# Kernel optimization log

Measured on AMD Instinct MI355X. Metric: run time of the kernel, lower is better.

Reference implementation:

```python
import jax, jax.numpy as jnp
import numpy as np

TEMPERATURE = 8.0  # sqrt(head_dim=64)
NEG_INF = -1000000000.0


def setup_inputs() -> dict:
    key = jax.random.key(0)
    kq, kk, kv, km = jax.random.split(key, 4)
    B, H, S, D = 2, 16, 2048, 64
    q = jax.random.normal(kq, (B, H, S, D), dtype=jnp.float32)
    k = jax.random.normal(kk, (B, H, S, D), dtype=jnp.float32)
    v = jax.random.normal(kv, (B, H, S, D), dtype=jnp.float32)
    mask = jax.random.randint(km, (B, 1, S, S), 0, 2, dtype=jnp.int32)
    return {"q": q, "k": k, "v": v, "mask": mask}


def reference(q, k, v, mask):
    # scores: [B,H,S,S] = (q/T) @ k^T
    attn = jnp.einsum('bhqd,bhkd->bhqk', q / TEMPERATURE, k)
    attn = jnp.where(mask == 0, NEG_INF, attn)
    attn = jax.nn.softmax(attn, axis=-1)  # dropout is identity in eval mode
    output = jnp.einsum('bhqk,bhkd->bhqd', attn, v)
    return (output, attn)
```

## Files before the change

### kernel.cpp

```cpp
#include <hip/hip_runtime.h>
#include <hip/hip_bf16.h>


using short4v = __attribute__((ext_vector_type(4))) short;
using short8v = __attribute__((ext_vector_type(8))) short;
using float4v = __attribute__((ext_vector_type(4))) float;

#define S_LEN 2048
#define D_DIM 64
#define QT 64
#define KTILE 64
#define NIT (S_LEN / KTILE)
#define NW (S_LEN / 64)
#define LDK 72
#define ATTN_OFF (2 * 16 * 2048 * 64)

__device__ __forceinline__ short f2bf(float x) {
  __hip_bfloat16 h = __float2bfloat16(x);
  return __builtin_bit_cast(short, h);
}
__device__ __forceinline__ float bf2f(short s) {
  return __builtin_bit_cast(float, ((unsigned)(unsigned short)s) << 16);
}

__global__ __launch_bounds__(256) void pack_mask_kernel(
    const int* __restrict__ mask, unsigned long long* __restrict__ pm, int nwords) {
  const int lane = threadIdx.x & 63;
  int gw = (blockIdx.x * blockDim.x + threadIdx.x) >> 6;
  const int stride = (gridDim.x * blockDim.x) >> 6;
  for (int w = gw; w < nwords; w += stride) {
    int m = mask[(size_t)w * 64 + lane];
    unsigned long long bits = __ballot(m != 0);
    if (lane == 0) pm[w] = bits;
  }
}

template <bool PACKED>
__global__ __launch_bounds__(256, 4) void sdpa_kernel(
    const float* __restrict__ q, const float* __restrict__ k,
    const float* __restrict__ v, const int* __restrict__ mask,
    const unsigned long long* __restrict__ pm, float* __restrict__ out) {
  __shared__ short lds_k[KTILE * LDK];
  __shared__ short lds_vt[D_DIM * LDK];
  __shared__ short lds_p[QT * LDK];

  const int tid  = threadIdx.x;
  const int wave = tid >> 6;
  const int lane = tid & 63;
  const int quad = lane >> 4;
  const int l16  = lane & 15;

  const int blk = blockIdx.x;
  const int qt  = blk & (NIT - 1);
  const int bh  = blk >> 5;
  const int b   = bh >> 4;

  const float* qp = q + (size_t)bh * S_LEN * D_DIM;
  const float* kp = k + (size_t)bh * S_LEN * D_DIM;
  const float* vp = v + (size_t)bh * S_LEN * D_DIM;
  const int*   mp = mask + (size_t)b * S_LEN * S_LEN;
  float* outO = out + (size_t)bh * S_LEN * D_DIM;
  float* outA = out + (size_t)ATTN_OFF + (size_t)bh * S_LEN * S_LEN;

  const int qbase = qt * QT;
  const int qrowC = qbase + wave * 16 + quad * 4;

  const float QSCALE = 0.18033688011112042f;
  short8v qa[2];
  {
    const int qrow = qbase + wave * 16 + l16;
    const float* src = qp + (size_t)qrow * D_DIM + quad * 8;
#pragma unroll
    for (int c = 0; c < 2; ++c) {
      float4v x0 = *(const float4v*)(src + c * 32);
      float4v x1 = *(const float4v*)(src + c * 32 + 4);
      short8v t;
      t[0] = f2bf(x0[0] * QSCALE); t[1] = f2bf(x0[1] * QSCALE);
      t[2] = f2bf(x0[2] * QSCALE); t[3] = f2bf(x0[3] * QSCALE);
      t[4] = f2bf(x1[0] * QSCALE); t[5] = f2bf(x1[1] * QSCALE);
      t[6] = f2bf(x1[2] * QSCALE); t[7] = f2bf(x1[3] * QSCALE);
      qa[c] = t;
    }
  }

  float lsum[4] = {0.f, 0.f, 0.f, 0.f};

#pragma unroll 1
  for (int kt = 0; kt < NIT; ++kt) {
#pragma unroll
    for (int i = 0; i < 4; ++i) {
      int f = tid + i * 256;
      int row = f >> 4;
      int col = (f & 15) * 4;
      float4v x = *(const float4v*)(kp + (size_t)(kt * KTILE + row) * D_DIM + col);
      short4v y;
      y[0] = f2bf(x[0]); y[1] = f2bf(x[1]); y[2] = f2bf(x[2]); y[3] = f2bf(x[3]);
      *(short4v*)(lds_k + row * LDK + col) = y;
    }
    __syncthreads();

    unsigned long long mrow[4];
    if (PACKED) {
#pragma unroll
      for (int r = 0; r < 4; ++r)
        mrow[r] = pm[((size_t)b * S_LEN + qrowC + r) * NW + kt];
    }
#pragma unroll
    for (int t = 0; t < 4; ++t) {
      float4v acc = {0.f, 0.f, 0.f, 0.f};
#pragma unroll
      for (int c = 0; c < 2; ++c) {
        short8v bf = *(const short8v*)(lds_k + (t * 16 + l16) * LDK + c * 32 + quad * 8);
        acc = __builtin_amdgcn_mfma_f32_16x16x32_bf16(qa[c], bf, acc, 0, 0, 0);
      }
      const int kcol = kt * KTILE + t * 16 + l16;
#pragma unroll
      for (int r = 0; r < 4; ++r) {
        bool mv = PACKED ? (((mrow[r] >> (t * 16 + l16)) & 1ull) != 0)
                         : (mp[(size_t)(qrowC + r) * S_LEN + kcol] != 0);
        float p = mv ? exp2f(acc[r]) : 0.f;
        lsum[r] += p;
      }
    }
    __syncthreads();
  }

  float invl[4];
#pragma unroll
  for (int r = 0; r < 4; ++r) {
    float s = lsum[r];
    s += __shfl_xor(s, 1);
    s += __shfl_xor(s, 2);
    s += __shfl_xor(s, 4);
    s += __shfl_xor(s, 8);
    invl[r] = 1.0f / s;
  }

  float4v oacc[4];
#pragma unroll
  for (int dt = 0; dt < 4; ++dt) oacc[dt] = (float4v){0.f, 0.f, 0.f, 0.f};

#pragma unroll 1
  for (int kt = 0; kt < NIT; ++kt) {
#pragma unroll
    for (int i = 0; i < 4; ++i) {
      int f = tid + i * 256;
      int row = f >> 4;
      int col = (f & 15) * 4;
      float4v x = *(const float4v*)(kp + (size_t)(kt * KTILE + row) * D_DIM + col);
      short4v y;
      y[0] = f2bf(x[0]); y[1] = f2bf(x[1]); y[2] = f2bf(x[2]); y[3] = f2bf(x[3]);
      *(short4v*)(lds_k + row * LDK + col) = y;
    }
    {
      const int d = tid & 63;
      const int krg = (tid >> 6) * 4;
#pragma unroll
      for (int i = 0; i < 4; ++i) {
        int kr0 = i * 16 + krg;
        short4v y;
#pragma unroll
        for (int j = 0; j < 4; ++j) {
          float x = vp[(size_t)(kt * KTILE + kr0 + j) * D_DIM + d];
          y[j] = f2bf(x);
        }
        *(short4v*)(lds_vt + d * LDK + kr0) = y;
      }
    }
    __syncthreads();

    unsigned long long mrow[4];
    if (PACKED) {
#pragma unroll
      for (int r = 0; r < 4; ++r)
        mrow[r] = pm[((size_t)b * S_LEN + qrowC + r) * NW + kt];
    }
#pragma unroll
    for (int t = 0; t < 4; ++t) {
      float4v acc = {0.f, 0.f, 0.f, 0.f};
#pragma unroll
      for (int c = 0; c < 2; ++c) {
        short8v bf = *(const short8v*)(lds_k + (t * 16 + l16) * LDK + c * 32 + quad * 8);
        acc = __builtin_amdgcn_mfma_f32_16x16x32_bf16(qa[c], bf, acc, 0, 0, 0);
      }
      const int kcol = kt * KTILE + t * 16 + l16;
      short* prow = lds_p + (wave * 16 + quad * 4) * LDK + t * 16 + l16;
#pragma unroll
      for (int r = 0; r < 4; ++r) {
        bool mv = PACKED ? (((mrow[r] >> (t * 16 + l16)) & 1ull) != 0)
                         : (mp[(size_t)(qrowC + r) * S_LEN + kcol] != 0);
        float p = mv ? exp2f(acc[r]) * invl[r] : 0.f;
        prow[r * LDK] = f2bf(p);
      }
    }

    {
      const int row16 = lane >> 2;
      const int cg = (lane & 3) * 16;
      const short* src = lds_p + (wave * 16 + row16) * LDK + cg;
      short8v p0 = *(const short8v*)src;
      short8v p1 = *(const short8v*)(src + 8);
      float* arow = outA + (size_t)(qbase + wave * 16 + row16) * S_LEN + kt * KTILE + cg;
      float4v f0 = {bf2f(p0[0]), bf2f(p0[1]), bf2f(p0[2]), bf2f(p0[3])};
      float4v f1 = {bf2f(p0[4]), bf2f(p0[5]), bf2f(p0[6]), bf2f(p0[7])};
      float4v f2 = {bf2f(p1[0]), bf2f(p1[1]), bf2f(p1[2]), bf2f(p1[3])};
      float4v f3 = {bf2f(p1[4]), bf2f(p1[5]), bf2f(p1[6]), bf2f(p1[7])};
      *(float4v*)(arow)      = f0;
      *(float4v*)(arow + 4)  = f1;
      *(float4v*)(arow + 8)  = f2;
      *(float4v*)(arow + 12) = f3;
    }

#pragma unroll
    for (int c = 0; c < 2; ++c) {
      short8v pa = *(const short8v*)(lds_p + (wave * 16 + l16) * LDK + c * 32 + quad * 8);
#pragma unroll
      for (int dt = 0; dt < 4; ++dt) {
        short8v vb = *(const short8v*)(lds_vt + (dt * 16 + l16) * LDK + c * 32 + quad * 8);
        oacc[dt] = __builtin_amdgcn_mfma_f32_16x16x32_bf16(pa, vb, oacc[dt], 0, 0, 0);
      }
    }
    __syncthreads();
  }

  {
    float* orow = outO + (size_t)qrowC * D_DIM + l16;
#pragma unroll
    for (int dt = 0; dt < 4; ++dt) {
#pragma unroll
      for (int r = 0; r < 4; ++r) {
        orow[(size_t)r * D_DIM + dt * 16] = oacc[dt][r];
      }
    }
  }
}

extern "C" void kernel_launch(void* const* d_in, const int* in_sizes, int n_in,
                              void* d_out, int out_size, void* d_ws, size_t ws_size,
                              hipStream_t stream) {
  const float* q = (const float*)d_in[0];
  const float* k = (const float*)d_in[1];
  const float* v = (const float*)d_in[2];
  const int* mask = (const int*)d_in[3];
  float* out = (float*)d_out;

  const int BH = 2 * 16;
  dim3 grid(BH * (S_LEN / QT));
  dim3 block(256);

  const int nwords = 2 * S_LEN * NW;
  const size_t pm_bytes = (size_t)nwords * 8;
  if (ws_size >= pm_bytes) {
    unsigned long long* pm = (unsigned long long*)d_ws;
    pack_mask_kernel<<<256, 256, 0, stream>>>(mask, pm, nwords);
    sdpa_kernel<true><<<grid, block, 0, stream>>>(q, k, v, mask, pm, out);
  } else {
    sdpa_kernel<false><<<grid, block, 0, stream>>>(q, k, v, mask, nullptr, out);
  }
}
```

Measured before the change: 844.8 us.

## Pre-convert K/V to swizzled bf16 and double-buffer tiles via global_load_lds

Adds prep kernels that convert K to bf16 and V to transposed bf16 once, in an XOR-swizzled tile layout in workspace. The main kernel then streams these tiles into double-buffered LDS with direct global-to-LDS loads, prefetching the next tile and mask words while computing the current one. It also remaps block indices so neighbouring blocks spread across heads. This removes the repeated per-block fp32 load and convert work for K/V, and the uncoalesced transposed V reads, at the cost of extra launches, more workspace, more LDS per block and a lower occupancy hint.

```diff
diff --git a/kernel.cpp b/kernel.cpp
--- a/kernel.cpp
+++ b/kernel.cpp
@@ -14,6 +14,10 @@
 #define NW (S_LEN / 64)
 #define LDK 72
 #define ATTN_OFF (2 * 16 * 2048 * 64)
+#define TILE_SH (KTILE * D_DIM)
+
+typedef __attribute__((address_space(1))) const unsigned int gu32;
+typedef __attribute__((address_space(3))) unsigned int lu32;
 
 __device__ __forceinline__ short f2bf(float x) {
   __hip_bfloat16 h = __float2bfloat16(x);
@@ -35,13 +39,63 @@
   }
 }
 
-template <bool PACKED>
-__global__ __launch_bounds__(256, 4) void sdpa_kernel(
-    const float* __restrict__ q, const float* __restrict__ k,
-    const float* __restrict__ v, const int* __restrict__ mask,
-    const unsigned long long* __restrict__ pm, float* __restrict__ out) {
-  __shared__ short lds_k[KTILE * LDK];
-  __shared__ short lds_vt[D_DIM * LDK];
+__global__ __launch_bounds__(256) void kprep_kernel(
+    const float* __restrict__ k, short* __restrict__ kbs) {
+  int g = blockIdx.x * 256 + threadIdx.x;
+  int kr = g >> 3;
+  int slot = g & 7;
+  const float* src = k + (size_t)kr * D_DIM + ((slot ^ (kr & 7)) << 3);
+  float4v a = *(const float4v*)src;
+  float4v b = *(const float4v*)(src + 4);
+  short8v t;
+  t[0] = f2bf(a[0]); t[1] = f2bf(a[1]); t[2] = f2bf(a[2]); t[3] = f2bf(a[3]);
+  t[4] = f2bf(b[0]); t[5] = f2bf(b[1]); t[6] = f2bf(b[2]); t[7] = f2bf(b[3]);
+  *(short8v*)(kbs + (size_t)g * 8) = t;
+}
+
+__global__ __launch_bounds__(256) void vprep_kernel(
+    const float* __restrict__ v, short* __restrict__ vts) {
+  __shared__ short lds_t[64 * 72];
+  const int tid = threadIdx.x;
+  const int bh = blockIdx.x >> 5;
+  const int kt = blockIdx.x & 31;
+  const float* vp = v + ((size_t)bh * S_LEN + kt * KTILE) * D_DIM;
+#pragma unroll
+  for (int i = 0; i < 4; ++i) {
+    int idx = tid + i * 256;
+    int s = idx >> 4;
+    int d0 = (idx & 15) * 4;
+    float4v x = *(const float4v*)(vp + (size_t)s * D_DIM + d0);
+#pragma unroll
+    for (int j = 0; j < 4; ++j) lds_t[(d0 + j) * 72 + s] = f2bf(x[j]);
+  }
+  __syncthreads();
+  short* dst = vts + (size_t)blockIdx.x * TILE_SH;
+#pragma unroll
+  for (int i = 0; i < 2; ++i) {
+    int g = tid + i * 256;
+    int d = g >> 3;
+    int slot = g & 7;
+    int lsrc = slot ^ (d & 7);
+    short8v t = *(const short8v*)(lds_t + d * 72 + lsrc * 8);
+    *(short8v*)(dst + g * 8) = t;
+  }
+}
+
+__device__ __forceinline__ void stage_wave(const short* __restrict__ g, short* l,
+                                           int wave, int lane) {
+  const short* s0 = g + wave * 1024 + lane * 8;
+  short* d0 = l + wave * 1024;
+  __builtin_amdgcn_global_load_lds((gu32*)s0, (lu32*)d0, 16, 0, 0);
+  __builtin_amdgcn_global_load_lds((gu32*)(s0 + 512), (lu32*)(d0 + 512), 16, 0, 0);
+}
+
+__global__ __launch_bounds__(256, 3) void sdpa_fused(
+    const float* __restrict__ q, const short* __restrict__ kbs,
+    const short* __restrict__ vts, const unsigned long long* __restrict__ pm,
+    float* __restrict__ out) {
+  __shared__ __align__(16) short lds_k[2][TILE_SH];
+  __shared__ __align__(16) short lds_vt[2][TILE_SH];
   __shared__ short lds_p[QT * LDK];
 
   const int tid  = threadIdx.x;
@@ -50,15 +104,14 @@
   const int quad = lane >> 4;
   const int l16  = lane & 15;
 
-  const int blk = blockIdx.x;
+  const int blk = (blockIdx.x & 7) * 128 + (blockIdx.x >> 3);
   const int qt  = blk & (NIT - 1);
   const int bh  = blk >> 5;
   const int b   = bh >> 4;
 
   const float* qp = q + (size_t)bh * S_LEN * D_DIM;
-  const float* kp = k + (size_t)bh * S_LEN * D_DIM;
-  const float* vp = v + (size_t)bh * S_LEN * D_DIM;
-  const int*   mp = mask + (size_t)b * S_LEN * S_LEN;
+  const short* kb_g = kbs + (size_t)bh * S_LEN * D_DIM;
+  const short* vt_g = vts + (size_t)bh * (NIT * TILE_SH);
   float* outO = out + (size_t)bh * S_LEN * D_DIM;
   float* outA = out + (size_t)ATTN_OFF + (size_t)bh * S_LEN * S_LEN;
 
@@ -83,45 +136,42 @@
     }
   }
 
+  const unsigned long long* pmrow = pm + ((size_t)b * S_LEN + qrowC) * NW;
+
   float lsum[4] = {0.f, 0.f, 0.f, 0.f};
+  unsigned long long mrow_c[4], mrow_n[4];
+#pragma unroll
+  for (int r = 0; r < 4; ++r) mrow_c[r] = pmrow[(size_t)r * NW];
+  stage_wave(kb_g, lds_k[0], wave, lane);
+  __syncthreads();
 
 #pragma unroll 1
   for (int kt = 0; kt < NIT; ++kt) {
-#pragma unroll
-    for (int i = 0; i < 4; ++i) {
-      int f = tid + i * 256;
-      int row = f >> 4;
-      int col = (f & 15) * 4;
-      float4v x = *(const float4v*)(kp + (size_t)(kt * KTILE + row) * D_DIM + col);
-      short4v y;
-      y[0] = f2bf(x[0]); y[1] = f2bf(x[1]); y[2] = f2bf(x[2]); y[3] = f2bf(x[3]);
-      *(short4v*)(lds_k + row * LDK + col) = y;
-    }
-    __syncthreads();
-
-    unsigned long long mrow[4];
-    if (PACKED) {
-#pragma unroll
-      for (int r = 0; r < 4; ++r)
-        mrow[r] = pm[((size_t)b * S_LEN + qrowC + r) * NW + kt];
-    }
+    if (kt + 1 < NIT) {
+#pragma unroll
+      for (int r = 0; r < 4; ++r) mrow_n[r] = pmrow[(size_t)r * NW + kt + 1];
+      stage_wave(kb_g + (kt + 1) * TILE_SH, lds_k[(kt + 1) & 1], wave, lane);
+    }
+    const short* kbuf = lds_k[kt & 1];
 #pragma unroll
     for (int t = 0; t < 4; ++t) {
       float4v acc = {0.f, 0.f, 0.f, 0.f};
+      const int row = t * 16 + l16;
+      const int sw = (row & 7) << 3;
 #pragma unroll
       for (int c = 0; c < 2; ++c) {
-        short8v bf = *(const short8v*)(lds_k + (t * 16 + l16) * LDK + c * 32 + quad * 8);
+        short8v bf = *(const short8v*)(kbuf + row * 64 + (((c * 32) + quad * 8) ^ sw));
         acc = __builtin_amdgcn_mfma_f32_16x16x32_bf16(qa[c], bf, acc, 0, 0, 0);
       }
-      const int kcol = kt * KTILE + t * 16 + l16;
 #pragma unroll
       for (int r = 0; r < 4; ++r) {
-        bool mv = PACKED ? (((mrow[r] >> (t * 16 + l16)) & 1ull) != 0)
-                         : (mp[(size_t)(qrowC + r) * S_LEN + kcol] != 0);
+        bool mv = ((mrow_c[r] >> (t * 16 + l16)) & 1ull) != 0;
         float p = mv ? exp2f(acc[r]) : 0.f;
         lsum[r] += p;
       }
     }
+#pragma unroll
+    for (int r = 0; r < 4; ++r) mrow_c[r] = mrow_n[r];
     __syncthreads();
   }
 
@@ -140,55 +190,37 @@
 #pragma unroll
   for (int dt = 0; dt < 4; ++dt) oacc[dt] = (float4v){0.f, 0.f, 0.f, 0.f};
 
+#pragma unroll
+  for (int r = 0; r < 4; ++r) mrow_c[r] = pmrow[(size_t)r * NW];
+  stage_wave(kb_g, lds_k[0], wave, lane);
+  stage_wave(vt_g, lds_vt[0], wave, lane);
+  __syncthreads();
+
 #pragma unroll 1
   for (int kt = 0; kt < NIT; ++kt) {
-#pragma unroll
-    for (int i = 0; i < 4; ++i) {
-      int f = tid + i * 256;
-      int row = f >> 4;
-      int col = (f & 15) * 4;
-      float4v x = *(const float4v*)(kp + (size_t)(kt * KTILE + row) * D_DIM + col);
-      short4v y;
-      y[0] = f2bf(x[0]); y[1] = f2bf(x[1]); y[2] = f2bf(x[2]); y[3] = f2bf(x[3]);
-      *(short4v*)(lds_k + row * LDK + col) = y;
-    }
-    {
-      const int d = tid & 63;
-      const int krg = (tid >> 6) * 4;
-#pragma unroll
-      for (int i = 0; i < 4; ++i) {
-        int kr0 = i * 16 + krg;
-        short4v y;
-#pragma unroll
-        for (int j = 0; j < 4; ++j) {
-          float x = vp[(size_t)(kt * KTILE + kr0 + j) * D_DIM + d];
-          y[j] = f2bf(x);
-        }
-        *(short4v*)(lds_vt + d * LDK + kr0) = y;
-      }
-    }
-    __syncthreads();
-
-    unsigned long long mrow[4];
-    if (PACKED) {
-#pragma unroll
-      for (int r = 0; r < 4; ++r)
-        mrow[r] = pm[((size_t)b * S_LEN + qrowC + r) * NW + kt];
-    }
+    if (kt + 1 < NIT) {
+#pragma unroll
+      for (int r = 0; r < 4; ++r) mrow_n[r] = pmrow[(size_t)r * NW + kt + 1];
+      stage_wave(kb_g + (kt + 1) * TILE_SH, lds_k[(kt + 1) & 1], wave, lane);
+      stage_wave(vt_g + (kt + 1) * TILE_SH, lds_vt[(kt + 1) & 1], wave, lane);
+    }
+    const short* kbuf = lds_k[kt & 1];
+    const short* vbuf = lds_vt[kt & 1];
+
 #pragma unroll
     for (int t = 0; t < 4; ++t) {
       float4v acc = {0.f, 0.f, 0.f, 0.f};
+      const int row = t * 16 + l16;
+      const int sw = (row & 7) << 3;
 #pragma unroll
       for (int c = 0; c < 2; ++c) {
-        short8v bf = *(const short8v*)(lds_k + (t * 16 + l16) * LDK + c * 32 + quad * 8);
+        short8v bf = *(const short8v*)(kbuf + row * 64 + (((c * 32) + quad * 8) ^ sw));
         acc = __builtin_amdgcn_mfma_f32_16x16x32_bf16(qa[c], bf, acc, 0, 0, 0);
       }
-      const int kcol = kt * KTILE + t * 16 + l16;
       short* prow = lds_p + (wave * 16 + quad * 4) * LDK + t * 16 + l16;
 #pragma unroll
       for (int r = 0; r < 4; ++r) {
-        bool mv = PACKED ? (((mrow[r] >> (t * 16 + l16)) & 1ull) != 0)
-                         : (mp[(size_t)(qrowC + r) * S_LEN + kcol] != 0);
+        bool mv = ((mrow_c[r] >> (t * 16 + l16)) & 1ull) != 0;
         float p = mv ? exp2f(acc[r]) * invl[r] : 0.f;
         prow[r * LDK] = f2bf(p);
       }
@@ -216,6 +248,210 @@
       short8v pa = *(const short8v*)(lds_p + (wave * 16 + l16) * LDK + c * 32 + quad * 8);
 #pragma unroll
       for (int dt = 0; dt < 4; ++dt) {
+        const int row = dt * 16 + l16;
+        const int sw = (row & 7) << 3;
+        short8v vb = *(const short8v*)(vbuf + row * 64 + (((c * 32) + quad * 8) ^ sw));
+        oacc[dt] = __builtin_amdgcn_mfma_f32_16x16x32_bf16(pa, vb, oacc[dt], 0, 0, 0);
+      }
+    }
+#pragma unroll
+    for (int r = 0; r < 4; ++r) mrow_c[r] = mrow_n[r];
+    __syncthreads();
+  }
+
+  {
+    float* orow = outO + (size_t)qrowC * D_DIM + l16;
+#pragma unroll
+    for (int dt = 0; dt < 4; ++dt) {
+#pragma unroll
+      for (int r = 0; r < 4; ++r) {
+        orow[(size_t)r * D_DIM + dt * 16] = oacc[dt][r];
+      }
+    }
+  }
+}
+
+template <bool PACKED>
+__global__ __launch_bounds__(256, 4) void sdpa_kernel(
+    const float* __restrict__ q, const float* __restrict__ k,
+    const float* __restrict__ v, const int* __restrict__ mask,
+    const unsigned long long* __restrict__ pm, float* __restrict__ out) {
+  __shared__ short lds_k[KTILE * LDK];
+  __shared__ short lds_vt[D_DIM * LDK];
+  __shared__ short lds_p[QT * LDK];
+
+  const int tid  = threadIdx.x;
+  const int wave = tid >> 6;
+  const int lane = tid & 63;
+  const int quad = lane >> 4;
+  const int l16  = lane & 15;
+
+  const int blk = blockIdx.x;
+  const int qt  = blk & (NIT - 1);
+  const int bh  = blk >> 5;
+  const int b   = bh >> 4;
+
+  const float* qp = q + (size_t)bh * S_LEN * D_DIM;
+  const float* kp = k + (size_t)bh * S_LEN * D_DIM;
+  const float* vp = v + (size_t)bh * S_LEN * D_DIM;
+  const int*   mp = mask + (size_t)b * S_LEN * S_LEN;
+  float* outO = out + (size_t)bh * S_LEN * D_DIM;
+  float* outA = out + (size_t)ATTN_OFF + (size_t)bh * S_LEN * S_LEN;
+
+  const int qbase = qt * QT;
+  const int qrowC = qbase + wave * 16 + quad * 4;
+
+  const float QSCALE = 0.18033688011112042f;
+  short8v qa[2];
+  {
+    const int qrow = qbase + wave * 16 + l16;
+    const float* src = qp + (size_t)qrow * D_DIM + quad * 8;
+#pragma unroll
+    for (int c = 0; c < 2; ++c) {
+      float4v x0 = *(const float4v*)(src + c * 32);
+      float4v x1 = *(const float4v*)(src + c * 32 + 4);
+      short8v t;
+      t[0] = f2bf(x0[0] * QSCALE); t[1] = f2bf(x0[1] * QSCALE);
+      t[2] = f2bf(x0[2] * QSCALE); t[3] = f2bf(x0[3] * QSCALE);
+      t[4] = f2bf(x1[0] * QSCALE); t[5] = f2bf(x1[1] * QSCALE);
+      t[6] = f2bf(x1[2] * QSCALE); t[7] = f2bf(x1[3] * QSCALE);
+      qa[c] = t;
+    }
+  }
+
+  float lsum[4] = {0.f, 0.f, 0.f, 0.f};
+
+#pragma unroll 1
+  for (int kt = 0; kt < NIT; ++kt) {
+#pragma unroll
+    for (int i = 0; i < 4; ++i) {
+      int f = tid + i * 256;
+      int row = f >> 4;
+      int col = (f & 15) * 4;
+      float4v x = *(const float4v*)(kp + (size_t)(kt * KTILE + row) * D_DIM + col);
+      short4v y;
+      y[0] = f2bf(x[0]); y[1] = f2bf(x[1]); y[2] = f2bf(x[2]); y[3] = f2bf(x[3]);
+      *(short4v*)(lds_k + row * LDK + col) = y;
+    }
+    __syncthreads();
+
+    unsigned long long mrow[4];
+    if (PACKED) {
+#pragma unroll
+      for (int r = 0; r < 4; ++r)
+        mrow[r] = pm[((size_t)b * S_LEN + qrowC + r) * NW + kt];
+    }
+#pragma unroll
+    for (int t = 0; t < 4; ++t) {
+      float4v acc = {0.f, 0.f, 0.f, 0.f};
+#pragma unroll
+      for (int c = 0; c < 2; ++c) {
+        short8v bf = *(const short8v*)(lds_k + (t * 16 + l16) * LDK + c * 32 + quad * 8);
+        acc = __builtin_amdgcn_mfma_f32_16x16x32_bf16(qa[c], bf, acc, 0, 0, 0);
+      }
+      const int kcol = kt * KTILE + t * 16 + l16;
+#pragma unroll
+      for (int r = 0; r < 4; ++r) {
+        bool mv = PACKED ? (((mrow[r] >> (t * 16 + l16)) & 1ull) != 0)
+                         : (mp[(size_t)(qrowC + r) * S_LEN + kcol] != 0);
+        float p = mv ? exp2f(acc[r]) : 0.f;
+        lsum[r] += p;
+      }
+    }
+    __syncthreads();
+  }
+
+  float invl[4];
+#pragma unroll
+  for (int r = 0; r < 4; ++r) {
+    float s = lsum[r];
+    s += __shfl_xor(s, 1);
+    s += __shfl_xor(s, 2);
+    s += __shfl_xor(s, 4);
+    s += __shfl_xor(s, 8);
+    invl[r] = 1.0f / s;
+  }
+
+  float4v oacc[4];
+#pragma unroll
+  for (int dt = 0; dt < 4; ++dt) oacc[dt] = (float4v){0.f, 0.f, 0.f, 0.f};
+
+#pragma unroll 1
+  for (int kt = 0; kt < NIT; ++kt) {
+#pragma unroll
+    for (int i = 0; i < 4; ++i) {
+      int f = tid + i * 256;
+      int row = f >> 4;
+      int col = (f & 15) * 4;
+      float4v x = *(const float4v*)(kp + (size_t)(kt * KTILE + row) * D_DIM + col);
+      short4v y;
+      y[0] = f2bf(x[0]); y[1] = f2bf(x[1]); y[2] = f2bf(x[2]); y[3] = f2bf(x[3]);
+      *(short4v*)(lds_k + row * LDK + col) = y;
+    }
+    {
+      const int d = tid & 63;
+      const int krg = (tid >> 6) * 4;
+#pragma unroll
+      for (int i = 0; i < 4; ++i) {
+        int kr0 = i * 16 + krg;
+        short4v y;
+#pragma unroll
+        for (int j = 0; j < 4; ++j) {
+          float x = vp[(size_t)(kt * KTILE + kr0 + j) * D_DIM + d];
+          y[j] = f2bf(x);
+        }
+        *(short4v*)(lds_vt + d * LDK + kr0) = y;
+      }
+    }
+    __syncthreads();
+
+    unsigned long long mrow[4];
+    if (PACKED) {
+#pragma unroll
+      for (int r = 0; r < 4; ++r)
+        mrow[r] = pm[((size_t)b * S_LEN + qrowC + r) * NW + kt];
+    }
+#pragma unroll
+    for (int t = 0; t < 4; ++t) {
+      float4v acc = {0.f, 0.f, 0.f, 0.f};
+#pragma unroll
+      for (int c = 0; c < 2; ++c) {
+        short8v bf = *(const short8v*)(lds_k + (t * 16 + l16) * LDK + c * 32 + quad * 8);
+        acc = __builtin_amdgcn_mfma_f32_16x16x32_bf16(qa[c], bf, acc, 0, 0, 0);
+      }
+      const int kcol = kt * KTILE + t * 16 + l16;
+      short* prow = lds_p + (wave * 16 + quad * 4) * LDK + t * 16 + l16;
+#pragma unroll
+      for (int r = 0; r < 4; ++r) {
+        bool mv = PACKED ? (((mrow[r] >> (t * 16 + l16)) & 1ull) != 0)
+                         : (mp[(size_t)(qrowC + r) * S_LEN + kcol] != 0);
+        float p = mv ? exp2f(acc[r]) * invl[r] : 0.f;
+        prow[r * LDK] = f2bf(p);
+      }
+    }
+
+    {
+      const int row16 = lane >> 2;
+      const int cg = (lane & 3) * 16;
+      const short* src = lds_p + (wave * 16 + row16) * LDK + cg;
+      short8v p0 = *(const short8v*)src;
+      short8v p1 = *(const short8v*)(src + 8);
+      float* arow = outA + (size_t)(qbase + wave * 16 + row16) * S_LEN + kt * KTILE + cg;
+      float4v f0 = {bf2f(p0[0]), bf2f(p0[1]), bf2f(p0[2]), bf2f(p0[3])};
+      float4v f1 = {bf2f(p0[4]), bf2f(p0[5]), bf2f(p0[6]), bf2f(p0[7])};
+      float4v f2 = {bf2f(p1[0]), bf2f(p1[1]), bf2f(p1[2]), bf2f(p1[3])};
+      float4v f3 = {bf2f(p1[4]), bf2f(p1[5]), bf2f(p1[6]), bf2f(p1[7])};
+      *(float4v*)(arow)      = f0;
+      *(float4v*)(arow + 4)  = f1;
+      *(float4v*)(arow + 8)  = f2;
+      *(float4v*)(arow + 12) = f3;
+    }
+
+#pragma unroll
+    for (int c = 0; c < 2; ++c) {
+      short8v pa = *(const short8v*)(lds_p + (wave * 16 + l16) * LDK + c * 32 + quad * 8);
+#pragma unroll
+      for (int dt = 0; dt < 4; ++dt) {
         short8v vb = *(const short8v*)(lds_vt + (dt * 16 + l16) * LDK + c * 32 + quad * 8);
         oacc[dt] = __builtin_amdgcn_mfma_f32_16x16x32_bf16(pa, vb, oacc[dt], 0, 0, 0);
       }
@@ -250,7 +486,20 @@
 
   const int nwords = 2 * S_LEN * NW;
   const size_t pm_bytes = (size_t)nwords * 8;
-  if (ws_size >= pm_bytes) {
+  const size_t kbs_bytes = (size_t)BH * S_LEN * D_DIM * 2;
+  const size_t kbs_off = pm_bytes;
+  const size_t vts_off = kbs_off + kbs_bytes;
+  const size_t need = vts_off + kbs_bytes;
+
+  if (ws_size >= need) {
+    unsigned long long* pm = (unsigned long long*)d_ws;
+    short* kbs = (short*)((char*)d_ws + kbs_off);
+    short* vts = (short*)((char*)d_ws + vts_off);
+    pack_mask_kernel<<<256, 256, 0, stream>>>(mask, pm, nwords);
+    kprep_kernel<<<2048, 256, 0, stream>>>(k, kbs);
+    vprep_kernel<<<1024, 256, 0, stream>>>(v, vts);
+    sdpa_fused<<<grid, block, 0, stream>>>(q, kbs, vts, pm, out);
+  } else if (ws_size >= pm_bytes) {
     unsigned long long* pm = (unsigned long long*)d_ws;
     pack_mask_kernel<<<256, 256, 0, stream>>>(mask, pm, nwords);
     sdpa_kernel<true><<<grid, block, 0, stream>>>(q, k, v, mask, pm, out);
```

Result: no change. 845.5 us (+0.1%).
